# Kernel optimization log

Hardware: AMD Instinct MI355X
Metric: run time of the kernel (lower is better)

## Reference

```python
import jax, jax.numpy as jnp
import numpy as np

BS, C1, NY, NX = 8, 64, 256, 256
C2, K, P = 64, 3, 1
N = 131072  # number of active (b, y, x) indices


def setup_inputs() -> dict:
    key = jax.random.key(0)
    k1, k2, k3, k4, k5, k6 = jax.random.split(key, 6)
    x = jax.random.normal(k1, (BS, C1, NY, NX), dtype=jnp.float32)
    bi = jax.random.randint(k2, (N,), 0, BS)
    yi = jax.random.randint(k3, (N,), 0, NY)
    xi = jax.random.randint(k4, (N,), 0, NX)
    indices = jnp.stack([bi, yi, xi], axis=1).astype(jnp.int32)
    weight = jax.random.normal(k5, (C2, C1, K, K), dtype=jnp.float32) * 0.05
    bias = jax.random.normal(k6, (C2,), dtype=jnp.float32) * 0.05
    return {"x": x, "indices": indices, "weight": weight, "bias": bias}


def reference(x, indices, weight, bias):
    # x: [bs, c1, ny, nx]; indices: [N, 3] of (b, y, x); weight: [c2, c1, k, k]
    bs, c1, ny, nx = x.shape
    c2, _, k, _ = weight.shape
    p = (k - 1) // 2  # asserted k == 2p + 1 in original
    xp = jnp.pad(x, ((0, 0), (0, 0), (p, p), (p, p)))  # zero-pad like F.unfold
    bi, yi, xi = indices[:, 0], indices[:, 1], indices[:, 2]
    dy = jnp.arange(k)
    dx = jnp.arange(k)
    rows = yi[:, None, None] + dy[None, :, None]  # [N, k, 1]
    cols = xi[:, None, None] + dx[None, None, :]  # [N, 1, k]
    # gather only active patches (equiv. to unfold[bi, yi, xi] in the original)
    # advanced indices at dims 0,2,3 -> result [N, k, k, c1]
    patches = xp[bi[:, None, None], :, rows, cols]
    # F.unfold channel ordering is (c1, kh, kw) flattened
    patches = patches.transpose(0, 3, 1, 2).reshape(patches.shape[0], c1 * k * k)
    w_flat = weight.reshape(c2, c1 * k * k)
    z = patches @ w_flat.T + bias  # [N, c2]
    return z
```

## Files before the change

### kernel.cpp

```cpp
#include <hip/hip_runtime.h>
#include <hip/hip_bf16.h>
#include <stdint.h>

#define NPTS 131072

typedef __attribute__((ext_vector_type(8))) short bf16x8;
typedef __attribute__((ext_vector_type(4))) float f32x4;
typedef __attribute__((ext_vector_type(8))) unsigned short u16x8;

__device__ inline unsigned short f32_to_bf16(float f) {
    union { __hip_bfloat16 h; unsigned short u; } cv;
    cv.h = __float2bfloat16(f);
    return cv.u;
}

__global__ __launch_bounds__(256) void k_prep(const float* __restrict__ x,
                                              unsigned short* __restrict__ xt,
                                              const float* __restrict__ w,
                                              unsigned short* __restrict__ wfrag) {
    if (blockIdx.x >= 2048) {
        int tid = (blockIdx.x - 2048) * 256 + threadIdx.x;
        int ci = tid >> 6;
        int l  = tid & 63;
        int q    = ci >> 3;
        int half = (ci >> 2) & 1;
        int nn   = ci & 3;
        int c2   = nn * 16 + (l & 15);
        int cin0 = half * 32 + ((l >> 4) << 3);
        u16x8 o;
#pragma unroll
        for (int e = 0; e < 8; ++e)
            o[e] = f32_to_bf16(w[c2 * 576 + (cin0 + e) * 9 + q]);
        *(u16x8*)(wfrag + tid * 8) = o;
        if (blockIdx.x == 2048 && threadIdx.x < 8) {
            u16x8 z = {};
            *(u16x8*)(xt + (size_t)8 * 65536 * 64 + threadIdx.x * 8) = z;
        }
        return;
    }

    __shared__ float tile[64][65];
    int batch   = blockIdx.x >> 8;
    int pixbase = (blockIdx.x & 255) << 8;
    int t = threadIdx.x;
    const float* xb = x + (size_t)batch * 64 * 65536;

    int c0  = t >> 4;
    int px4 = (t & 15) << 2;
    int c8  = (t & 7) << 3;
    int pp  = t >> 3;

    for (int sub = 0; sub < 4; ++sub) {
        int pix0 = pixbase + (sub << 6);
        if (sub) __syncthreads();
#pragma unroll
        for (int i = 0; i < 4; ++i) {
            int c = c0 + i * 16;
            float4 v = *(const float4*)(xb + (size_t)c * 65536 + pix0 + px4);
            tile[c][px4 + 0] = v.x; tile[c][px4 + 1] = v.y;
            tile[c][px4 + 2] = v.z; tile[c][px4 + 3] = v.w;
        }
        __syncthreads();
#pragma unroll
        for (int h = 0; h < 2; ++h) {
            int pix = pp + h * 32;
            u16x8 o;
#pragma unroll
            for (int i = 0; i < 8; ++i) o[i] = f32_to_bf16(tile[c8 + i][pix]);
            *(u16x8*)(xt + ((size_t)(batch * 65536 + pix0 + pix) * 64 + c8)) = o;
        }
    }
}

__global__ __launch_bounds__(512, 4) void k_gather_gemm(
    const unsigned short* __restrict__ xt,
    const unsigned short* __restrict__ wfrag,
    const int* __restrict__ indices,
    const float* __restrict__ bias,
    float* __restrict__ out) {
    __shared__ unsigned short wlds[72 * 512];

    int t = threadIdx.x;
    int w = t >> 6;
    int l = t & 63;
    int lo = l & 15;
    int hi = l >> 4;

#pragma unroll
    for (int i = 0; i < 9; ++i) {
        int m = t + i * 512;
        *(u16x8*)(&wlds[m * 8]) = *(const u16x8*)(wfrag + m * 8);
    }

    int pt = blockIdx.x * 128 + w * 16 + lo;
    int b  = indices[pt * 3 + 0];
    int yi = indices[pt * 3 + 1];
    int xi = indices[pt * 3 + 2];

    const uint32_t PADOFF = (uint32_t)8 * 65536 * 128;
    uint32_t sub = (uint32_t)(hi << 4);

    uint32_t off[9];
#pragma unroll
    for (int q = 0; q < 9; ++q) {
        int yy = yi + (q / 3) - 1;
        int xx = xi + (q % 3) - 1;
        bool v = ((unsigned)yy < 256u) & ((unsigned)xx < 256u);
        uint32_t pix = ((uint32_t)b << 16) + ((uint32_t)(yy & 255) << 8) + (uint32_t)(xx & 255);
        off[q] = (v ? pix * 128u : PADOFF) + sub;
    }

    bf16x8 a[18];
#pragma unroll
    for (int q = 0; q < 9; ++q) {
        a[2 * q + 0] = (bf16x8)(*(const u16x8*)((const char*)xt + off[q]));
        a[2 * q + 1] = (bf16x8)(*(const u16x8*)((const char*)xt + off[q] + 64));
    }

    f32x4 acc[4];
#pragma unroll
    for (int nn = 0; nn < 4; ++nn) acc[nn] = (f32x4)0.0f;

    __syncthreads();

#pragma unroll
    for (int q = 0; q < 9; ++q) {
#pragma unroll
        for (int h = 0; h < 2; ++h) {
            const unsigned short* base = &wlds[q * 4096 + h * 2048];
#pragma unroll
            for (int nn = 0; nn < 4; ++nn) {
                bf16x8 bf = *(const bf16x8*)(base + nn * 512 + l * 8);
                acc[nn] = __builtin_amdgcn_mfma_f32_16x16x32_bf16(a[2 * q + h], bf, acc[nn], 0, 0, 0);
            }
        }
    }

    int rbase = blockIdx.x * 128 + w * 16 + (hi << 2);
#pragma unroll
    for (int nn = 0; nn < 4; ++nn) {
        float bv = bias[nn * 16 + lo];
#pragma unroll
        for (int r = 0; r < 4; ++r) {
            out[(size_t)(rbase + r) * 64 + nn * 16 + lo] = acc[nn][r] + bv;
        }
    }
}

__global__ void k_naive(const float* __restrict__ x, const int* __restrict__ idx,
                        const float* __restrict__ w, const float* __restrict__ bias,
                        float* __restrict__ out) {
    int i = blockIdx.x * 256 + threadIdx.x;
    if (i >= NPTS * 64) return;
    int p = i >> 6, c2 = i & 63;
    int b = idx[p * 3], yi = idx[p * 3 + 1], xi = idx[p * 3 + 2];
    float acc = bias[c2];
    for (int c = 0; c < 64; ++c) {
        const float* xp = x + ((size_t)(b * 64 + c) << 16);
        const float* wp = w + (c2 * 64 + c) * 9;
        for (int dy = 0; dy < 3; ++dy) {
            int yy = yi + dy - 1;
            if ((unsigned)yy >= 256u) continue;
            for (int dx = 0; dx < 3; ++dx) {
                int xx = xi + dx - 1;
                if ((unsigned)xx >= 256u) continue;
                acc += xp[(yy << 8) + xx] * wp[dy * 3 + dx];
            }
        }
    }
    out[i] = acc;
}

extern "C" void kernel_launch(void* const* d_in, const int* in_sizes, int n_in,
                              void* d_out, int out_size, void* d_ws, size_t ws_size,
                              hipStream_t stream) {
    const float* x       = (const float*)d_in[0];
    const int*   indices = (const int*)d_in[1];
    const float* weight  = (const float*)d_in[2];
    const float* bias    = (const float*)d_in[3];
    float* out = (float*)d_out;

    size_t xt_bytes = (size_t)8 * 65536 * 64 * 2 + 128;
    size_t need = xt_bytes + (size_t)72 * 1024;
    if (ws_size < need) {
        k_naive<<<(NPTS * 64 + 255) / 256, 256, 0, stream>>>(x, indices, weight, bias, out);
        return;
    }
    unsigned short* xt    = (unsigned short*)d_ws;
    unsigned short* wfrag = (unsigned short*)((char*)d_ws + xt_bytes);

    k_prep<<<2048 + 18, 256, 0, stream>>>(x, xt, weight, wfrag);
    k_gather_gemm<<<NPTS / 128, 512, 0, stream>>>(xt, wfrag, indices, bias, out);
}
```

Baseline: 65.60 us.

## Bin active points by spatial tile before gather-GEMM for locality

```diff
diff --git a/kernel.cpp b/kernel.cpp
--- a/kernel.cpp
+++ b/kernel.cpp
@@ -3,6 +3,7 @@
 #include <stdint.h>
 
 #define NPTS 131072
+#define NBINS 2048
 
 typedef __attribute__((ext_vector_type(8))) short bf16x8;
 typedef __attribute__((ext_vector_type(4))) float f32x4;
@@ -17,8 +18,15 @@
 __global__ __launch_bounds__(256) void k_prep(const float* __restrict__ x,
                                               unsigned short* __restrict__ xt,
                                               const float* __restrict__ w,
-                                              unsigned short* __restrict__ wfrag) {
+                                              unsigned short* __restrict__ wfrag,
+                                              int* __restrict__ hist) {
     if (blockIdx.x >= 2048) {
+        if (blockIdx.x == 2066) {
+#pragma unroll
+            for (int i = 0; i < NBINS / 256; ++i)
+                hist[threadIdx.x + i * 256] = 0;
+            return;
+        }
         int tid = (blockIdx.x - 2048) * 256 + threadIdx.x;
         int ci = tid >> 6;
         int l  = tid & 63;
@@ -72,10 +80,51 @@
     }
 }
 
+__device__ inline int point_key(int b, int y, int x) {
+    return (b << 8) | ((y >> 4) << 4) | (x >> 4);
+}
+
+__global__ __launch_bounds__(256) void k_hist(const int* __restrict__ indices,
+                                              int* __restrict__ hist) {
+    int p = blockIdx.x * 256 + threadIdx.x;
+    int b = indices[p * 3], y = indices[p * 3 + 1], x = indices[p * 3 + 2];
+    atomicAdd(&hist[point_key(b, y, x)], 1);
+}
+
+__global__ __launch_bounds__(256) void k_scan(const int* __restrict__ hist,
+                                              int* __restrict__ cursor) {
+    __shared__ int tsum[256];
+    int t = threadIdx.x;
+    int local[8];
+    int s = 0;
+#pragma unroll
+    for (int i = 0; i < 8; ++i) { local[i] = hist[t * 8 + i]; s += local[i]; }
+    tsum[t] = s;
+    __syncthreads();
+    for (int off = 1; off < 256; off <<= 1) {
+        int u = (t >= off) ? tsum[t - off] : 0;
+        __syncthreads();
+        tsum[t] += u;
+        __syncthreads();
+    }
+    int running = tsum[t] - s;
+#pragma unroll
+    for (int i = 0; i < 8; ++i) { cursor[t * 8 + i] = running; running += local[i]; }
+}
+
+__global__ __launch_bounds__(256) void k_scatter(const int* __restrict__ indices,
+                                                 int* __restrict__ cursor,
+                                                 int4* __restrict__ sorted) {
+    int p = blockIdx.x * 256 + threadIdx.x;
+    int b = indices[p * 3], y = indices[p * 3 + 1], x = indices[p * 3 + 2];
+    int slot = atomicAdd(&cursor[point_key(b, y, x)], 1);
+    sorted[slot] = make_int4(b, y, x, p);
+}
+
 __global__ __launch_bounds__(512, 4) void k_gather_gemm(
     const unsigned short* __restrict__ xt,
     const unsigned short* __restrict__ wfrag,
-    const int* __restrict__ indices,
+    const int4* __restrict__ sorted,
     const float* __restrict__ bias,
     float* __restrict__ out) {
     __shared__ unsigned short wlds[72 * 512];
@@ -86,16 +135,17 @@
     int lo = l & 15;
     int hi = l >> 4;
 
+    int sb = (blockIdx.x & 7) * 128 + (blockIdx.x >> 3);
+
 #pragma unroll
     for (int i = 0; i < 9; ++i) {
         int m = t + i * 512;
         *(u16x8*)(&wlds[m * 8]) = *(const u16x8*)(wfrag + m * 8);
     }
 
-    int pt = blockIdx.x * 128 + w * 16 + lo;
-    int b  = indices[pt * 3 + 0];
-    int yi = indices[pt * 3 + 1];
-    int xi = indices[pt * 3 + 2];
+    int slot = sb * 128 + w * 16 + lo;
+    int4 s4 = sorted[slot];
+    int b = s4.x, yi = s4.y, xi = s4.z;
 
     const uint32_t PADOFF = (uint32_t)8 * 65536 * 128;
     uint32_t sub = (uint32_t)(hi << 4);
@@ -136,13 +186,16 @@
         }
     }
 
-    int rbase = blockIdx.x * 128 + w * 16 + (hi << 2);
+    int slotbase = sb * 128 + w * 16 + (hi << 2);
+    int pt[4];
+#pragma unroll
+    for (int r = 0; r < 4; ++r) pt[r] = sorted[slotbase + r].w;
 #pragma unroll
     for (int nn = 0; nn < 4; ++nn) {
         float bv = bias[nn * 16 + lo];
 #pragma unroll
         for (int r = 0; r < 4; ++r) {
-            out[(size_t)(rbase + r) * 64 + nn * 16 + lo] = acc[nn][r] + bv;
+            out[(size_t)pt[r] * 64 + nn * 16 + lo] = acc[nn][r] + bv;
         }
     }
 }
@@ -180,15 +233,26 @@
     const float* bias    = (const float*)d_in[3];
     float* out = (float*)d_out;
 
-    size_t xt_bytes = (size_t)8 * 65536 * 64 * 2 + 128;
-    size_t need = xt_bytes + (size_t)72 * 1024;
+    size_t xt_bytes     = (size_t)8 * 65536 * 64 * 2 + 128;
+    size_t wfrag_bytes  = (size_t)72 * 1024;
+    size_t hist_bytes   = (size_t)NBINS * 4;
+    size_t cursor_bytes = (size_t)NBINS * 4;
+    size_t sorted_bytes = (size_t)NPTS * 16;
+    size_t need = xt_bytes + wfrag_bytes + hist_bytes + cursor_bytes + sorted_bytes;
     if (ws_size < need) {
         k_naive<<<(NPTS * 64 + 255) / 256, 256, 0, stream>>>(x, indices, weight, bias, out);
         return;
     }
-    unsigned short* xt    = (unsigned short*)d_ws;
-    unsigned short* wfrag = (unsigned short*)((char*)d_ws + xt_bytes);
-
-    k_prep<<<2048 + 18, 256, 0, stream>>>(x, xt, weight, wfrag);
-    k_gather_gemm<<<NPTS / 128, 512, 0, stream>>>(xt, wfrag, indices, bias, out);
-}
+    char* p = (char*)d_ws;
+    unsigned short* xt    = (unsigned short*)p;  p += xt_bytes;
+    unsigned short* wfrag = (unsigned short*)p;  p += wfrag_bytes;
+    int*            hist  = (int*)p;             p += hist_bytes;
+    int*            cursor= (int*)p;             p += cursor_bytes;
+    int4*           sorted= (int4*)p;
+
+    k_prep<<<2048 + 18 + 1, 256, 0, stream>>>(x, xt, weight, wfrag, hist);
+    k_hist<<<NPTS / 256, 256, 0, stream>>>(indices, hist);
+    k_scan<<<1, 256, 0, stream>>>(hist, cursor);
+    k_scatter<<<NPTS / 256, 256, 0, stream>>>(indices, cursor, sorted);
+    k_gather_gemm<<<NPTS / 128, 512, 0, stream>>>(xt, wfrag, sorted, bias, out);
+}
```

Measured after the change: 98.68 us. +50.4%, slower.
